# Kernel optimization log

Hardware: AMD Instinct MI355X
Metric: run time of the kernel (lower is better)

The kernel has to match this reference:

```python
import jax, jax.numpy as jnp
import numpy as np

TEMPERATURE = 0.07
EPS = 1e-12  # F.normalize clamp


def _project(x, We, be, W1, b1, W2, b2):
    # encoder Linear then projection head Linear->ReLU->Linear
    h = x @ We + be                      # [B, 512]
    h = jax.nn.relu(h @ W1 + b1)         # [B, 256]
    return h @ W2 + b2                   # [B, 128]


def _ntxent(z1, z2, t):
    B = z1.shape[0]
    z1 = z1 / jnp.maximum(jnp.linalg.norm(z1, axis=1, keepdims=True), EPS)
    z2 = z2 / jnp.maximum(jnp.linalg.norm(z2, axis=1, keepdims=True), EPS)
    reps = jnp.concatenate([z1, z2], axis=0)          # [2B, 128]
    sim = reps @ reps.T                               # [2B, 2B]
    N = 2 * B
    idx = jnp.arange(N)
    # positives: eye rolled by B along columns -> column (i+B) mod N
    pos = sim[idx, (idx + B) % N][:, None]            # [N, 1]
    # negatives: all off-diagonal entries per row, in column order
    cols = jnp.arange(N - 1)[None, :]                 # [1, N-1]
    neg_idx = cols + (cols >= idx[:, None])           # skip the diagonal
    neg = jnp.take_along_axis(sim, neg_idx, axis=1)   # [N, N-1]
    logits = jnp.concatenate([pos, neg], axis=1) / t  # [N, N]
    # cross-entropy with label 0
    return jnp.mean(jax.nn.logsumexp(logits, axis=1) - logits[:, 0])


def setup_inputs() -> dict:
    key = jax.random.key(0)
    ks = jax.random.split(key, 10)
    B, Din, Denc, Dh, Dp = 4096, 1024, 512, 256, 128
    s = lambda fan_in: 1.0 / np.sqrt(fan_in)
    return {
        "x_image": jax.random.normal(ks[0], (B, Din), jnp.float32),
        "x_text": jax.random.normal(ks[1], (B, Din), jnp.float32),
        "We_img": jax.random.normal(ks[2], (Din, Denc), jnp.float32) * s(Din),
        "be_img": jnp.zeros((Denc,), jnp.float32),
        "We_txt": jax.random.normal(ks[3], (Din, Denc), jnp.float32) * s(Din),
        "be_txt": jnp.zeros((Denc,), jnp.float32),
        "Wp1_img": jax.random.normal(ks[4], (Denc, Dh), jnp.float32) * s(Denc),
        "bp1_img": jnp.zeros((Dh,), jnp.float32),
        "Wp2_img": jax.random.normal(ks[5], (Dh, Dp), jnp.float32) * s(Dh),
        "bp2_img": jnp.zeros((Dp,), jnp.float32),
        "Wp1_txt": jax.random.normal(ks[6], (Denc, Dh), jnp.float32) * s(Denc),
        "bp1_txt": jnp.zeros((Dh,), jnp.float32),
        "Wp2_txt": jax.random.normal(ks[7], (Dh, Dp), jnp.float32) * s(Dh),
        "bp2_txt": jnp.zeros((Dp,), jnp.float32),
    }


def reference(x_image, x_text, We_img, be_img, We_txt, be_txt,
              Wp1_img, bp1_img, Wp2_img, bp2_img,
              Wp1_txt, bp1_txt, Wp2_txt, bp2_txt):
    z1 = _project(x_image, We_img, be_img, Wp1_img, bp1_img, Wp2_img, bp2_img)
    z2 = _project(x_text, We_txt, be_txt, Wp1_txt, bp1_txt, Wp2_txt, bp2_txt)
    # single modality pair ('image','text') -> one NT-Xent loss
    return _ntxent(z1, z2, TEMPERATURE)
```

## Files before the change

### kernel.cpp

```cpp
#include <hip/hip_runtime.h>
#include <hip/hip_bf16.h>
#include <math.h>

typedef __bf16 bf16_t;
typedef __bf16 bf8 __attribute__((ext_vector_type(8)));
typedef __bf16 bf4 __attribute__((ext_vector_type(4)));
typedef float f32x4 __attribute__((ext_vector_type(4)));
typedef int i32x8 __attribute__((ext_vector_type(8)));
typedef unsigned char u8;

#define AS1 __attribute__((address_space(1)))
#define AS3 __attribute__((address_space(3)))

#define B_ROWS 4096
#define NTOT   8192
#define DIN    1024
#define DENC   512
#define DH     256
#define DP     128
#define NSLICE 32
#define INV_T        14.285714285714286f
#define SCALE_LOG2   20.609929155556620f

__device__ __forceinline__ f32x4 mfma_16x16x32(bf8 a, bf8 b, f32x4 c) {
  return __builtin_amdgcn_mfma_f32_16x16x32_bf16(a, b, c, 0, 0, 0);
}

__global__ __launch_bounds__(256) void prep_kernel(
    const float* __restrict__ x_i, const float* __restrict__ x_t,
    const float* __restrict__ We_i, const float* __restrict__ We_t,
    const float* __restrict__ W1_i, const float* __restrict__ W1_t,
    const float* __restrict__ W2_i, const float* __restrict__ W2_t,
    bf16_t* __restrict__ xb_i, bf16_t* __restrict__ xb_t,
    bf16_t* __restrict__ Wet_i, bf16_t* __restrict__ Wet_t,
    bf16_t* __restrict__ W1t_i, bf16_t* __restrict__ W1t_t,
    bf16_t* __restrict__ W2t_i, bf16_t* __restrict__ W2t_t) {
  const int b = blockIdx.x;
  const int tid = threadIdx.x;
  if (b >= 336) {
    int idx = (b - 336) * 256 + tid;
    const int HALF = (B_ROWS * DIN) / 4;
    const float* s; bf16_t* d; int off;
    if (idx < HALF) { s = x_i; d = xb_i; off = idx; }
    else            { s = x_t; d = xb_t; off = idx - HALF; }
    float4 v = ((const float4*)s)[off];
    bf4 w = { (bf16_t)v.x, (bf16_t)v.y, (bf16_t)v.z, (bf16_t)v.w };
    ((bf4*)d)[off] = w;
    return;
  }
  const float* src; bf16_t* dst; int K, N, tile;
  if (b < 128)      { src = We_i; dst = Wet_i; K = 1024; N = 512; tile = b; }
  else if (b < 256) { src = We_t; dst = Wet_t; K = 1024; N = 512; tile = b - 128; }
  else if (b < 288) { src = W1_i; dst = W1t_i; K = 512;  N = 256; tile = b - 256; }
  else if (b < 320) { src = W1_t; dst = W1t_t; K = 512;  N = 256; tile = b - 288; }
  else if (b < 328) { src = W2_i; dst = W2t_i; K = 256;  N = 128; tile = b - 320; }
  else              { src = W2_t; dst = W2t_t; K = 256;  N = 128; tile = b - 328; }
  const int tilesN = N >> 6;
  const int k0 = (tile / tilesN) * 64;
  const int n0 = (tile % tilesN) * 64;

  __shared__ float ld[64][65];
  #pragma unroll
  for (int i = 0; i < 4; ++i) {
    int cid = tid + i * 256;
    int r = cid >> 4;
    int c = (cid & 15) * 4;
    float4 v = *(const float4*)(src + (size_t)(k0 + r) * N + n0 + c);
    ld[r][c + 0] = v.x; ld[r][c + 1] = v.y; ld[r][c + 2] = v.z; ld[r][c + 3] = v.w;
  }
  __syncthreads();
  #pragma unroll
  for (int i = 0; i < 2; ++i) {
    int cid = tid + i * 256;
    int rn = cid >> 3;
    int c8 = (cid & 7) * 8;
    bf8 w;
    #pragma unroll
    for (int j = 0; j < 8; ++j) w[j] = (bf16_t)ld[c8 + j][rn];
    *(bf8*)(dst + (size_t)(n0 + rn) * K + k0 + c8) = w;
  }
}

template<int MT, bool RELU>
__global__ __launch_bounds__(256) void gemm_glds(
    const bf16_t* __restrict__ A0, const bf16_t* __restrict__ A1,
    const bf16_t* __restrict__ B0, const bf16_t* __restrict__ B1,
    const float* __restrict__ bias0, const float* __restrict__ bias1,
    bf16_t* __restrict__ out0, bf16_t* __restrict__ out1,
    int N, int K) {
  const bf16_t* A   = blockIdx.z ? A1 : A0;
  const bf16_t* Bt  = blockIdx.z ? B1 : B0;
  const float* bias = blockIdx.z ? bias1 : bias0;
  bf16_t* outp      = blockIdx.z ? out1 : out0;

  const int nb   = blockIdx.x * 64;
  const int mb   = blockIdx.y * MT;
  const int tid  = threadIdx.x;
  const int wave = tid >> 6;
  const int lane = tid & 63;
  const int l15  = lane & 15;
  const int quad = lane >> 4;
  constexpr int CH = MT / 64;

  __shared__ __align__(16) bf16_t As[2][MT * 32];
  __shared__ __align__(16) bf16_t Bs[2][64 * 32];

  f32x4 acc[CH][4];
  #pragma unroll
  for (int i = 0; i < CH; ++i)
    #pragma unroll
    for (int j = 0; j < 4; ++j) acc[i][j] = (f32x4){0.f, 0.f, 0.f, 0.f};

  auto stage = [&](int k0, int pb) {
    #pragma unroll
    for (int i = 0; i < CH; ++i) {
      const int s = tid + i * 256;
      const bf16_t* ga = A + (size_t)(mb + (s >> 2)) * K + k0 + (s & 3) * 8;
      __builtin_amdgcn_global_load_lds(
          (const AS1 void*)ga,
          (AS3 void*)(As[pb] + (size_t)(wave * 64 + i * 256) * 8), 16, 0, 0);
    }
    const bf16_t* gb = Bt + (size_t)(nb + (tid >> 2)) * K + k0 + (tid & 3) * 8;
    __builtin_amdgcn_global_load_lds(
        (const AS1 void*)gb,
        (AS3 void*)(Bs[pb] + (size_t)(wave * 64) * 8), 16, 0, 0);
  };

  stage(0, 0);
  const int T = K >> 5;
  for (int t = 0; t < T; ++t) {
    __syncthreads();
    if (t + 1 < T) stage((t + 1) << 5, (t + 1) & 1);
    const bf16_t* as = As[t & 1];
    const bf16_t* bs = Bs[t & 1];
    bf8 a[CH];
    #pragma unroll
    for (int i = 0; i < CH; ++i)
      a[i] = *(const bf8*)(as + (size_t)(wave * (16 * CH) + i * 16 + l15) * 32 + quad * 8);
    #pragma unroll
    for (int nt = 0; nt < 4; ++nt) {
      bf8 bb = *(const bf8*)(bs + (size_t)(nt * 16 + l15) * 32 + quad * 8);
      #pragma unroll
      for (int i = 0; i < CH; ++i)
        acc[i][nt] = mfma_16x16x32(a[i], bb, acc[i][nt]);
    }
  }

  #pragma unroll
  for (int i = 0; i < CH; ++i) {
    const int orow = mb + wave * (16 * CH) + i * 16 + quad * 4;
    #pragma unroll
    for (int nt = 0; nt < 4; ++nt) {
      const int ocol = nb + nt * 16 + l15;
      const float bval = bias[ocol];
      #pragma unroll
      for (int r = 0; r < 4; ++r) {
        float v = acc[i][nt][r] + bval;
        if (RELU) v = fmaxf(v, 0.f);
        outp[(size_t)(orow + r) * N + ocol] = (bf16_t)v;
      }
    }
  }
}

__global__ __launch_bounds__(256) void head2_norm(
    const bf16_t* __restrict__ A0, const bf16_t* __restrict__ A1,
    const bf16_t* __restrict__ B0, const bf16_t* __restrict__ B1,
    const float* __restrict__ bias0, const float* __restrict__ bias1,
    u8* __restrict__ reps8) {
  const bf16_t* A   = blockIdx.z ? A1 : A0;
  const bf16_t* Bt  = blockIdx.z ? B1 : B0;
  const float* bias = blockIdx.z ? bias1 : bias0;

  const int mb   = blockIdx.x * 16;
  const int tid  = threadIdx.x;
  const int wave = tid >> 6;
  const int lane = tid & 63;
  const int l15  = lane & 15;
  const int quad = lane >> 4;
  const int wc0  = wave * 32;

  __shared__ __align__(16) bf16_t Asb[2][16 * 32];
  __shared__ __align__(16) bf16_t Bsb[2][128 * 32];
  __shared__ float ssL[64];

  f32x4 acc[2];
  acc[0] = (f32x4){0.f, 0.f, 0.f, 0.f};
  acc[1] = (f32x4){0.f, 0.f, 0.f, 0.f};

  auto stage = [&](int k0, int pb) {
    if (wave == 0) {
      const int row = lane >> 2, j = lane & 3, cf = j ^ (row & 3);
      const bf16_t* ga = A + (size_t)(mb + row) * DH + k0 + cf * 8;
      __builtin_amdgcn_global_load_lds(
          (const AS1 void*)ga, (AS3 void*)(Asb[pb]), 16, 0, 0);
    }
    #pragma unroll
    for (int i = 0; i < 2; ++i) {
      const int s = wave * 64 + i * 256 + lane;
      const int col = s >> 2, j = s & 3, cf = j ^ (col & 3);
      const bf16_t* gb = Bt + (size_t)col * DH + k0 + cf * 8;
      __builtin_amdgcn_global_load_lds(
          (const AS1 void*)gb,
          (AS3 void*)(Bsb[pb] + (size_t)(wave * 64 + i * 256) * 8), 16, 0, 0);
    }
  };

  stage(0, 0);
  for (int t = 0; t < 8; ++t) {
    __syncthreads();
    if (t < 7) stage((t + 1) << 5, (t + 1) & 1);
    const bf16_t* as = Asb[t & 1];
    const bf16_t* bs = Bsb[t & 1];
    bf8 a = *(const bf8*)(as + (size_t)(l15 * 4 + (quad ^ (l15 & 3))) * 8);
    #pragma unroll
    for (int nt = 0; nt < 2; ++nt) {
      const int col = wc0 + nt * 16 + l15;
      bf8 bb = *(const bf8*)(bs + (size_t)(col * 4 + (quad ^ (col & 3))) * 8);
      acc[nt] = mfma_16x16x32(a, bb, acc[nt]);
    }
  }

  float ssp[4];
  #pragma unroll
  for (int r = 0; r < 4; ++r) {
    #pragma unroll
    for (int nt = 0; nt < 2; ++nt) acc[nt][r] += bias[wc0 + nt * 16 + l15];
    float s = acc[0][r] * acc[0][r] + acc[1][r] * acc[1][r];
    s += __shfl_xor(s, 1); s += __shfl_xor(s, 2);
    s += __shfl_xor(s, 4); s += __shfl_xor(s, 8);
    ssp[r] = s;
  }
  if (l15 == 0) {
    #pragma unroll
    for (int r = 0; r < 4; ++r) ssL[wave * 16 + quad * 4 + r] = ssp[r];
  }
  __syncthreads();
  const size_t gr0 = (size_t)(blockIdx.z ? B_ROWS : 0) + mb + quad * 4;
  #pragma unroll
  for (int r = 0; r < 4; ++r) {
    const int row = quad * 4 + r;
    float tot = ssL[row] + ssL[16 + row] + ssL[32 + row] + ssL[48 + row];
    const float inv = 1.0f / fmaxf(sqrtf(tot), 1e-12f);
    int pk = __builtin_amdgcn_cvt_pk_fp8_f32(acc[0][r] * inv, acc[1][r] * inv, 0, 0);
    reps8[(gr0 + r) * DP + wc0 + l15]      = (u8)(pk & 0xff);
    reps8[(gr0 + r) * DP + wc0 + 16 + l15] = (u8)((pk >> 8) & 0xff);
  }
}

__global__ __launch_bounds__(256) void sim_fp8_kernel(
    const u8* __restrict__ reps8, float* __restrict__ Spart) {
  const int rowbase = blockIdx.y * 256;
  const int slice   = blockIdx.x;
  const int col0    = slice * 256;
  const int tid  = threadIdx.x;
  const int wave = tid >> 6;
  const int lane = tid & 63;
  const int l15  = lane & 15;
  const int quad = lane >> 4;

  __shared__ __align__(16) u8 Bs[2][64 * DP];

  const int r0 = rowbase + wave * 64;
  i32x8 af[4];
  #pragma unroll
  for (int c = 0; c < 4; ++c) {
    const uint4* ap = (const uint4*)(reps8 + (size_t)(r0 + c * 16 + l15) * DP + quad * 32);
    uint4 x0 = ap[0], x1 = ap[1];
    af[c] = (i32x8){(int)x0.x, (int)x0.y, (int)x0.z, (int)x0.w,
                    (int)x1.x, (int)x1.y, (int)x1.z, (int)x1.w};
  }

  float rs[4][4];
  #pragma unroll
  for (int c = 0; c < 4; ++c)
    #pragma unroll
    for (int r = 0; r < 4; ++r) rs[c][r] = 0.f;

  auto stage = [&](int t, int pb) {
    const int jt0 = col0 + t * 64;
    #pragma unroll
    for (int i = 0; i < 2; ++i) {
      const int s   = i * 256 + tid;
      const int col = s >> 3;
      const int cf  = (s & 7) ^ (col & 7);
      const u8* g = reps8 + (size_t)(jt0 + col) * DP + cf * 16;
      __builtin_amdgcn_global_load_lds(
          (const AS1 void*)g,
          (AS3 void*)(Bs[pb] + (size_t)(i * 256 + wave * 64) * 16), 16, 0, 0);
    }
  };

  stage(0, 0);
  for (int t = 0; t < 4; ++t) {
    __syncthreads();
    if (t + 1 < 4) stage(t + 1, (t + 1) & 1);
    const u8* buf = Bs[t & 1];

    #pragma unroll
    for (int st = 0; st < 4; ++st) {
      const int coln = st * 16 + l15;
      const u8* cbase = buf + (size_t)coln * DP;
      const int c0 = ((2 * quad)     ^ (coln & 7)) * 16;
      const int c1 = ((2 * quad + 1) ^ (coln & 7)) * 16;
      uint4 b0 = *(const uint4*)(cbase + c0);
      uint4 b1 = *(const uint4*)(cbase + c1);
      i32x8 bf = (i32x8){(int)b0.x, (int)b0.y, (int)b0.z, (int)b0.w,
                         (int)b1.x, (int)b1.y, (int)b1.z, (int)b1.w};
      #pragma unroll
      for (int c = 0; c < 4; ++c) {
        f32x4 acc = (f32x4){0.f, 0.f, 0.f, 0.f};
        acc = __builtin_amdgcn_mfma_scale_f32_16x16x128_f8f6f4(
            af[c], bf, acc, 0, 0, 0, 0x7F7F7F7F, 0, 0x7F7F7F7F);
        #pragma unroll
        for (int r = 0; r < 4; ++r)
          rs[c][r] += __builtin_amdgcn_exp2f(acc[r] * SCALE_LOG2);
      }
    }
  }

  #pragma unroll
  for (int c = 0; c < 4; ++c) {
    const int i0 = r0 + c * 16 + quad * 4;
    #pragma unroll
    for (int r = 0; r < 4; ++r) {
      float v = rs[c][r];
      v += __shfl_xor(v, 1); v += __shfl_xor(v, 2);
      v += __shfl_xor(v, 4); v += __shfl_xor(v, 8);
      if (l15 == 0) Spart[(size_t)slice * NTOT + i0 + r] = v;
    }
  }
}

__global__ __launch_bounds__(256) void rowfinal_kernel(
    const u8* __restrict__ reps8, const float* __restrict__ Spart,
    float* __restrict__ L) {
  const int tid  = threadIdx.x;
  const int wave = tid >> 6;
  const int lane = tid & 63;
  const int row  = blockIdx.x * 4 + wave;
  const int ua = *(const unsigned short*)(reps8 + (size_t)row * DP + lane * 2);
  const int ub = *(const unsigned short*)(reps8 + (size_t)(row ^ B_ROWS) * DP + lane * 2);
  float a0 = __builtin_amdgcn_cvt_f32_fp8(ua, 0);
  float a1 = __builtin_amdgcn_cvt_f32_fp8(ua, 1);
  float b0 = __builtin_amdgcn_cvt_f32_fp8(ub, 0);
  float b1 = __builtin_amdgcn_cvt_f32_fp8(ub, 1);
  float dii = a0 * a0 + a1 * a1;
  float pos = a0 * b0 + a1 * b1;
  float ps  = (lane < NSLICE) ? Spart[(size_t)lane * NTOT + row] : 0.f;
  #pragma unroll
  for (int m = 1; m < 64; m <<= 1) {
    dii += __shfl_xor(dii, m);
    pos += __shfl_xor(pos, m);
    ps  += __shfl_xor(ps, m);
  }
  if (lane == 0) {
    float Si = ps - __builtin_amdgcn_exp2f(dii * SCALE_LOG2)
                  + __builtin_amdgcn_exp2f(pos * SCALE_LOG2);
    L[row] = logf(Si) - pos * INV_T;
  }
}

__global__ __launch_bounds__(1024) void reduce_kernel(
    const float* __restrict__ L, float* __restrict__ out) {
  const int tid = threadIdx.x;
  float acc = 0.f;
  for (int i = tid; i < NTOT; i += 1024) acc += L[i];
  #pragma unroll
  for (int m = 1; m < 64; m <<= 1) acc += __shfl_xor(acc, m);
  __shared__ float wsum[16];
  if ((tid & 63) == 0) wsum[tid >> 6] = acc;
  __syncthreads();
  if (tid < 16) {
    float v = wsum[tid];
    #pragma unroll
    for (int m = 1; m < 16; m <<= 1) v += __shfl_xor(v, m);
    if (tid == 0) out[0] = v * (1.0f / NTOT);
  }
}

extern "C" void kernel_launch(void* const* d_in, const int* in_sizes, int n_in,
                              void* d_out, int out_size, void* d_ws, size_t ws_size,
                              hipStream_t stream) {
  const float* x_img  = (const float*)d_in[0];
  const float* x_txt  = (const float*)d_in[1];
  const float* We_img = (const float*)d_in[2];
  const float* be_img = (const float*)d_in[3];
  const float* We_txt = (const float*)d_in[4];
  const float* be_txt = (const float*)d_in[5];
  const float* W1_img = (const float*)d_in[6];
  const float* b1_img = (const float*)d_in[7];
  const float* W2_img = (const float*)d_in[8];
  const float* b2_img = (const float*)d_in[9];
  const float* W1_txt = (const float*)d_in[10];
  const float* b1_txt = (const float*)d_in[11];
  const float* W2_txt = (const float*)d_in[12];
  const float* b2_txt = (const float*)d_in[13];

  char* p = (char*)d_ws;
  bf16_t* xbf_img = (bf16_t*)p; p += (size_t)B_ROWS * DIN * 2;
  bf16_t* xbf_txt = (bf16_t*)p; p += (size_t)B_ROWS * DIN * 2;
  bf16_t* Wet_img = (bf16_t*)p; p += (size_t)DENC * DIN * 2;
  bf16_t* Wet_txt = (bf16_t*)p; p += (size_t)DENC * DIN * 2;
  bf16_t* W1t_img = (bf16_t*)p; p += (size_t)DH * DENC * 2;
  bf16_t* W1t_txt = (bf16_t*)p; p += (size_t)DH * DENC * 2;
  bf16_t* W2t_img = (bf16_t*)p; p += (size_t)DP * DH * 2;
  bf16_t* W2t_txt = (bf16_t*)p; p += (size_t)DP * DH * 2;
  bf16_t* h_img   = (bf16_t*)p; p += (size_t)B_ROWS * DENC * 2;
  bf16_t* h_txt   = (bf16_t*)p; p += (size_t)B_ROWS * DENC * 2;
  bf16_t* g_img   = (bf16_t*)p; p += (size_t)B_ROWS * DH * 2;
  bf16_t* g_txt   = (bf16_t*)p; p += (size_t)B_ROWS * DH * 2;
  u8*     reps8   = (u8*)    p; p += (size_t)NTOT * DP;
  float*  Spart   = (float*) p; p += (size_t)NSLICE * NTOT * 4;
  float*  L       = (float*) p; p += (size_t)NTOT * 4;

  prep_kernel<<<336 + 8192, 256, 0, stream>>>(
      x_img, x_txt, We_img, We_txt, W1_img, W1_txt, W2_img, W2_txt,
      xbf_img, xbf_txt, Wet_img, Wet_txt, W1t_img, W1t_txt, W2t_img, W2t_txt);

  gemm_glds<128, false><<<dim3(DENC / 64, B_ROWS / 128, 2), 256, 0, stream>>>(
      xbf_img, xbf_txt, Wet_img, Wet_txt, be_img, be_txt, h_img, h_txt,
      DENC, DIN);
  gemm_glds<64, true><<<dim3(DH / 64, B_ROWS / 64, 2), 256, 0, stream>>>(
      h_img, h_txt, W1t_img, W1t_txt, b1_img, b1_txt, g_img, g_txt,
      DH, DENC);
  head2_norm<<<dim3(B_ROWS / 16, 1, 2), 256, 0, stream>>>(
      g_img, g_txt, W2t_img, W2t_txt, b2_img, b2_txt, reps8);

  sim_fp8_kernel<<<dim3(NSLICE, NTOT / 256), 256, 0, stream>>>(reps8, Spart);
  rowfinal_kernel<<<NTOT / 4, 256, 0, stream>>>(reps8, Spart, L);
  reduce_kernel<<<1, 1024, 0, stream>>>(L, (float*)d_out);
}
```

Measured before the change: 178.4 us.

## Exploit similarity matrix symmetry by computing only upper-triangular tiles

The similarity kernel now skips blocks below the diagonal. Each off-diagonal tile also sums its exponentials along columns and writes those sums as the row partials for the mirrored tile. This roughly halves the MFMA and exp work. In exchange it adds cross-lane shuffles, a shared-memory column reduction, and idle early-exit blocks in the launch grid.

```diff
diff --git a/kernel.cpp b/kernel.cpp
--- a/kernel.cpp
+++ b/kernel.cpp
@@ -250,9 +250,12 @@
 
 __global__ __launch_bounds__(256) void sim_fp8_kernel(
     const u8* __restrict__ reps8, float* __restrict__ Spart) {
-  const int rowbase = blockIdx.y * 256;
-  const int slice   = blockIdx.x;
-  const int col0    = slice * 256;
+  const int bx = blockIdx.x;
+  const int by = blockIdx.y;
+  if (bx < by) return;
+  const bool diag = (bx == by);
+  const int rowbase = by * 256;
+  const int col0    = bx * 256;
   const int tid  = threadIdx.x;
   const int wave = tid >> 6;
   const int lane = tid & 63;
@@ -260,6 +263,7 @@
   const int quad = lane >> 4;
 
   __shared__ __align__(16) u8 Bs[2][64 * DP];
+  __shared__ float csw[4][256];
 
   const int r0 = rowbase + wave * 64;
   i32x8 af[4];
@@ -307,14 +311,23 @@
       uint4 b1 = *(const uint4*)(cbase + c1);
       i32x8 bf = (i32x8){(int)b0.x, (int)b0.y, (int)b0.z, (int)b0.w,
                          (int)b1.x, (int)b1.y, (int)b1.z, (int)b1.w};
+      float cs = 0.f;
       #pragma unroll
       for (int c = 0; c < 4; ++c) {
         f32x4 acc = (f32x4){0.f, 0.f, 0.f, 0.f};
         acc = __builtin_amdgcn_mfma_scale_f32_16x16x128_f8f6f4(
             af[c], bf, acc, 0, 0, 0, 0x7F7F7F7F, 0, 0x7F7F7F7F);
         #pragma unroll
-        for (int r = 0; r < 4; ++r)
-          rs[c][r] += __builtin_amdgcn_exp2f(acc[r] * SCALE_LOG2);
+        for (int r = 0; r < 4; ++r) {
+          float ev = __builtin_amdgcn_exp2f(acc[r] * SCALE_LOG2);
+          rs[c][r] += ev;
+          cs += ev;
+        }
+      }
+      if (!diag) {
+        cs += __shfl_xor(cs, 16);
+        cs += __shfl_xor(cs, 32);
+        if (quad == 0) csw[wave][t * 64 + st * 16 + l15] = cs;
       }
     }
   }
@@ -327,8 +340,14 @@
       float v = rs[c][r];
       v += __shfl_xor(v, 1); v += __shfl_xor(v, 2);
       v += __shfl_xor(v, 4); v += __shfl_xor(v, 8);
-      if (l15 == 0) Spart[(size_t)slice * NTOT + i0 + r] = v;
-    }
+      if (l15 == 0) Spart[(size_t)bx * NTOT + i0 + r] = v;
+    }
+  }
+
+  if (!diag) {
+    __syncthreads();
+    float v = csw[0][tid] + csw[1][tid] + csw[2][tid] + csw[3][tid];
+    Spart[(size_t)by * NTOT + col0 + tid] = v;
   }
 }
 
```

New measurement: 192.1 us. 7.6% more time.
